# Kernel tuning notes

Measured on AMD Instinct MI355X. Metric: run time of the kernel, lower is better.

## Reference

```python
import jax, jax.numpy as jnp
import numpy as np

D_IN = 4096
D_OUT = 4096
RANK = 16
ALPHA = 32
SCALE = ALPHA / RANK


def setup_inputs() -> dict:
    key = jax.random.key(0)
    k_x, k_w, k_b, k_a = jax.random.split(key, 4)
    x = jax.random.normal(k_x, (4, 2048, D_IN), dtype=jnp.float32)
    weight = jax.random.normal(k_w, (D_OUT, D_IN), dtype=jnp.float32) * (1.0 / np.sqrt(D_IN))
    bias = jax.random.normal(k_b, (D_OUT,), dtype=jnp.float32)
    lora_A = jax.random.normal(k_a, (RANK, D_IN), dtype=jnp.float32) * 0.01
    lora_B = jnp.zeros((D_OUT, RANK), dtype=jnp.float32)
    return {"x": x, "weight": weight, "bias": bias, "lora_A": lora_A, "lora_B": lora_B}


def reference(x, weight, bias, lora_A, lora_B):
    # base linear: y = x @ W^T + b   -> [B, S, D_OUT]
    orig_out = jnp.einsum("bsd,od->bso", x, weight) + bias
    # low-rank path: (x @ A^T) @ B^T * (alpha/rank)
    lora_out = jnp.einsum("bsr,or->bso", jnp.einsum("bsd,rd->bsr", x, lora_A), lora_B)
    return orig_out + lora_out * SCALE
```

## Files before the change

### kernel.cpp

```cpp
#include <hip/hip_runtime.h>
#include <stdint.h>

#define DIN   4096
#define DOUT  4096
#define RANK  16
#define MTOT  8192
#define LSCALE 2.0f

typedef unsigned short u16;
typedef __bf16 bf16x8 __attribute__((ext_vector_type(8)));
typedef float  f32x4  __attribute__((ext_vector_type(4)));
typedef u16    u16x8  __attribute__((ext_vector_type(8)));

__device__ __forceinline__ u16 f2bf(float f) {
    uint32_t u = __builtin_bit_cast(uint32_t, f);
    u = (u + 0x7FFFu + ((u >> 16) & 1u)) >> 16;
    return (u16)u;
}

__device__ __forceinline__ u16x8 pack8(f32x4 a, f32x4 b) {
    u16x8 o;
    o[0] = f2bf(a[0]); o[1] = f2bf(a[1]); o[2] = f2bf(a[2]); o[3] = f2bf(a[3]);
    o[4] = f2bf(b[0]); o[5] = f2bf(b[1]); o[6] = f2bf(b[2]); o[7] = f2bf(b[3]);
    return o;
}

#define GLDS16(g, l) __builtin_amdgcn_global_load_lds( \
    (const __attribute__((address_space(1))) void*)(g), \
    (__attribute__((address_space(3))) void*)(l), 16, 0, 0)

__global__ __launch_bounds__(256) void k_convert_x(const float* __restrict__ x,
                                                   u16* __restrict__ xb) {
    long i = ((long)blockIdx.x * 256 + threadIdx.x) * 8;
    f32x4 a = *(const f32x4*)(x + i);
    f32x4 b = *(const f32x4*)(x + i + 4);
    *(u16x8*)(xb + i) = pack8(a, b);
}

__global__ __launch_bounds__(256) void k_build_weff(const float* __restrict__ W,
                                                    const float* __restrict__ A,
                                                    const float* __restrict__ B,
                                                    u16* __restrict__ wb) {
    long t = (long)blockIdx.x * 256 + threadIdx.x;
    long i = t * 8;
    int o = (int)(i >> 12);
    int d = (int)(i & (DIN - 1));
    float sB[RANK];
#pragma unroll
    for (int r = 0; r < RANK; ++r) sB[r] = B[o * RANK + r] * LSCALE;
    f32x4 w0 = *(const f32x4*)(W + i);
    f32x4 w1 = *(const f32x4*)(W + i + 4);
#pragma unroll
    for (int r = 0; r < RANK; ++r) {
        f32x4 a0 = *(const f32x4*)(A + (long)r * DIN + d);
        f32x4 a1 = *(const f32x4*)(A + (long)r * DIN + d + 4);
        w0 += a0 * sB[r];
        w1 += a1 * sB[r];
    }
    *(u16x8*)(wb + i) = pack8(w0, w1);
}

#define BM 256
#define BN 256
#define BK 64
#define NT (DIN / BK)

#define MFMA16(d, a, b) d = __builtin_amdgcn_mfma_f32_16x16x32_bf16(a, b, d, 0, 0, 0)
#define ABAR()   asm volatile("s_barrier" ::: "memory")
#define GATE4()  asm volatile("s_waitcnt vmcnt(4)" ::: "memory")
#define PRIO1()  __builtin_amdgcn_s_setprio(1)
#define PRIO0()  __builtin_amdgcn_s_setprio(0)

#define QUADK(mo, no, AF, BF) \
    _Pragma("unroll") \
    for (int kk = 0; kk < 2; ++kk) { \
        _Pragma("unroll") \
        for (int m = 0; m < 4; ++m) { \
            _Pragma("unroll") \
            for (int n = 0; n < 2; ++n) { \
                MFMA16(acc[(mo)+m][(no)+n], AF[m][kk], BF[n][kk]); \
            } \
        } \
    }

__global__ __launch_bounds__(512, 2) void k_gemm_ws(const u16* __restrict__ xb,
                                                    const u16* __restrict__ wb,
                                                    const float* __restrict__ bias,
                                                    float* __restrict__ out) {
    constexpr int K = DIN, N = DOUT;
    __shared__ alignas(16) u16 lds[65536];

    const int nchunk = gridDim.x >> 3;
    const int bid = blockIdx.x;
    const int wg  = (bid & 7) * nchunk + (bid >> 3);
    const int bm  = (wg & 31) * BM;
    const int bn  = (wg >> 5) * BN;

    const int tid  = threadIdx.x;
    const int lane = tid & 63;
    const int wid  = tid >> 6;
    const int wr   = wid >> 2;
    const int wc   = wid & 3;
    const int lrow = lane & 15;
    const int kgrp = lane >> 4;

    const int srow = tid >> 3;
    const int sgl  = (tid & 7) ^ (srow & 7);
    const u16* const aSrcB = xb + (long)(bm + srow) * K + sgl * 8;
    const u16* const bSrcB = wb + (long)(bn + srow) * K + sgl * 8;

#define STAGE_A(c, buf, kt) GLDS16(aSrcB + (long)(64*(c))*K + (kt)*BK, \
                                   lds + (buf)*16384 + (c)*4096 + tid*8)
#define STAGE_B(c, buf, kt) GLDS16(bSrcB + (long)(64*(c))*K + (kt)*BK, \
                                   lds + 32768 + (buf)*16384 + (c)*4096 + tid*8)

    const int go0 = (kgrp ^ (lrow & 7)) * 8;
    const int go1 = go0 ^ 32;
    const int arow = (wr*128 + lrow) * 64;
    const int brow = (wc*64  + lrow) * 64;

    f32x4 acc[8][4];
#pragma unroll
    for (int m = 0; m < 8; ++m)
#pragma unroll
        for (int n = 0; n < 4; ++n) acc[m][n] = (f32x4){0.f, 0.f, 0.f, 0.f};

    bf16x8 afL[4][2], afH[4][2], bfLo[2][2], bfHi[2][2];

    STAGE_A(0, 0, 0); STAGE_A(1, 0, 0);
    STAGE_A(2, 0, 0); STAGE_A(3, 0, 0);
    STAGE_B(0, 0, 0); STAGE_B(1, 0, 0);
    STAGE_B(2, 0, 0); STAGE_B(3, 0, 0);
    STAGE_B(0, 1, 1); STAGE_B(1, 1, 1);
    STAGE_B(2, 1, 1); STAGE_B(3, 1, 1);
    GATE4();
    __syncthreads();
#pragma unroll
    for (int nf = 0; nf < 2; ++nf) {
        const u16* b = lds + 32768 + brow + nf * 1024;
        bfLo[nf][0] = *(const bf16x8*)(b + go0);
        bfLo[nf][1] = *(const bf16x8*)(b + go1);
    }

    for (int t = 0; t < NT; ++t) {
        const int cur = t & 1, nxt = cur ^ 1;
        const int kt1 = (t + 1) & (NT - 1);
        const int kt2 = (t + 2) & (NT - 1);
        const u16* const cA = lds + cur * 16384;
        const u16* const cB = lds + 32768 + cur * 16384;
        const u16* const nB = lds + 32768 + nxt * 16384;

        STAGE_A(0, nxt, kt1); STAGE_A(1, nxt, kt1);
#pragma unroll
        for (int mf = 0; mf < 4; ++mf) {
            const u16* b = cA + arow + mf * 1024;
            afL[mf][0] = *(const bf16x8*)(b + go0);
            afL[mf][1] = *(const bf16x8*)(b + go1);
        }
        PRIO1(); QUADK(0, 0, afL, bfLo); PRIO0();
        ABAR();

        STAGE_A(2, nxt, kt1); STAGE_A(3, nxt, kt1);
#pragma unroll
        for (int nf = 0; nf < 2; ++nf) {
            const u16* b = cB + brow + (nf + 2) * 1024;
            bfHi[nf][0] = *(const bf16x8*)(b + go0);
            bfHi[nf][1] = *(const bf16x8*)(b + go1);
        }
        PRIO1(); QUADK(0, 2, afL, bfHi); PRIO0();
        ABAR();

        STAGE_B(0, cur, kt2); STAGE_B(1, cur, kt2);
#pragma unroll
        for (int mf = 0; mf < 4; ++mf) {
            const u16* b = cA + arow + (mf + 4) * 1024;
            afH[mf][0] = *(const bf16x8*)(b + go0);
            afH[mf][1] = *(const bf16x8*)(b + go1);
        }
        PRIO1(); QUADK(4, 0, afH, bfLo); PRIO0();
        ABAR();

        STAGE_B(2, cur, kt2); STAGE_B(3, cur, kt2);
        GATE4();
#pragma unroll
        for (int nf = 0; nf < 2; ++nf) {
            const u16* b = nB + brow + nf * 1024;
            bfLo[nf][0] = *(const bf16x8*)(b + go0);
            bfLo[nf][1] = *(const bf16x8*)(b + go1);
        }
        PRIO1(); QUADK(4, 2, afH, bfHi); PRIO0();
        ABAR();
    }
    asm volatile("s_waitcnt vmcnt(0)" ::: "memory");

    const int orow = bm + wr*128 + kgrp*4;
    const int ocol = bn + wc*64 + lrow;
#pragma unroll
    for (int n = 0; n < 4; ++n) {
        const int col = ocol + n*16;
        const float bj = bias[col];
#pragma unroll
        for (int m = 0; m < 8; ++m) {
            const int row = orow + m*16;
#pragma unroll
            for (int r = 0; r < 4; ++r)
                out[(long)(row + r) * N + col] = acc[m][n][r] + bj;
        }
    }
}

__global__ __launch_bounds__(64) void k_lora_T(const float* __restrict__ x,
                                               const float* __restrict__ A,
                                               float* __restrict__ T) {
    const int m = blockIdx.x;
    const int lane = threadIdx.x;
    const float* xr = x + (long)m * DIN;
    float acc[RANK];
#pragma unroll
    for (int r = 0; r < RANK; ++r) acc[r] = 0.f;
    for (int k = lane * 4; k < DIN; k += 64 * 4) {
        f32x4 xv = *(const f32x4*)(xr + k);
#pragma unroll
        for (int r = 0; r < RANK; ++r) {
            f32x4 av = *(const f32x4*)(A + (long)r * DIN + k);
            acc[r] += xv[0] * av[0] + xv[1] * av[1] + xv[2] * av[2] + xv[3] * av[3];
        }
    }
#pragma unroll
    for (int r = 0; r < RANK; ++r)
        for (int off = 32; off > 0; off >>= 1) acc[r] += __shfl_down(acc[r], off);
    if (lane == 0) {
#pragma unroll
        for (int r = 0; r < RANK; ++r) T[(long)m * RANK + r] = acc[r] * LSCALE;
    }
}

__global__ __launch_bounds__(256) void k_gemm_nows(const float* __restrict__ x,
                                                   const float* __restrict__ W,
                                                   const float* __restrict__ bias,
                                                   const float* __restrict__ T,
                                                   const float* __restrict__ lB,
                                                   float* __restrict__ out) {
    constexpr int FBM = 128, FBN = 128, FBK = 32, K = DIN, N = DOUT;
    __shared__ __align__(16) u16 As[FBM * FBK];
    __shared__ __align__(16) u16 Bs[FBN * FBK];

    const int tid = threadIdx.x;
    const int bm = blockIdx.y * FBM;
    const int bn = blockIdx.x * FBN;
    const int lane = tid & 63;
    const int wid  = tid >> 6;
    const int wr = wid >> 1, wc = wid & 1;
    const int lrow = lane & 15;
    const int kgrp = lane >> 4;

    const int c0 = tid, c1 = tid + 256;
    const float* aS0 = x + (long)(bm + (c0 >> 2)) * K + (c0 & 3) * 8;
    const float* aS1 = x + (long)(bm + (c1 >> 2)) * K + (c1 & 3) * 8;
    const float* bS0 = W + (long)(bn + (c0 >> 2)) * K + (c0 & 3) * 8;
    const float* bS1 = W + (long)(bn + (c1 >> 2)) * K + (c1 & 3) * 8;
    u16* aD0 = As + c0 * 8;  u16* aD1 = As + c1 * 8;
    u16* bD0 = Bs + c0 * 8;  u16* bD1 = Bs + c1 * 8;

    const u16* aR = As + (wr * 64 + lrow) * FBK + kgrp * 8;
    const u16* bR = Bs + (wc * 64 + lrow) * FBK + kgrp * 8;

    f32x4 acc[4][4];
#pragma unroll
    for (int i = 0; i < 4; ++i)
#pragma unroll
        for (int j = 0; j < 4; ++j) acc[i][j] = (f32x4){0.f, 0.f, 0.f, 0.f};

    for (int k0 = 0; k0 < K; k0 += FBK) {
        f32x4 a00 = *(const f32x4*)aS0, a01 = *(const f32x4*)(aS0 + 4);
        f32x4 a10 = *(const f32x4*)aS1, a11 = *(const f32x4*)(aS1 + 4);
        f32x4 b00 = *(const f32x4*)bS0, b01 = *(const f32x4*)(bS0 + 4);
        f32x4 b10 = *(const f32x4*)bS1, b11 = *(const f32x4*)(bS1 + 4);
        aS0 += FBK; aS1 += FBK; bS0 += FBK; bS1 += FBK;
        if (k0) __syncthreads();
        *(u16x8*)aD0 = pack8(a00, a01);
        *(u16x8*)aD1 = pack8(a10, a11);
        *(u16x8*)bD0 = pack8(b00, b01);
        *(u16x8*)bD1 = pack8(b10, b11);
        __syncthreads();

        bf16x8 af[4], bf[4];
#pragma unroll
        for (int i = 0; i < 4; ++i) af[i] = *(const bf16x8*)(aR + i * 16 * FBK);
#pragma unroll
        for (int j = 0; j < 4; ++j) bf[j] = *(const bf16x8*)(bR + j * 16 * FBK);
#pragma unroll
        for (int i = 0; i < 4; ++i)
#pragma unroll
            for (int j = 0; j < 4; ++j)
                acc[i][j] = __builtin_amdgcn_mfma_f32_16x16x32_bf16(af[i], bf[j], acc[i][j], 0, 0, 0);
    }

#pragma unroll
    for (int j = 0; j < 4; ++j) {
        const int col = bn + wc * 64 + j * 16 + lrow;
        const float bj = bias[col];
        float bl[RANK];
#pragma unroll
        for (int q = 0; q < RANK; ++q) bl[q] = lB[(long)col * RANK + q];
#pragma unroll
        for (int i = 0; i < 4; ++i) {
            const int row0 = bm + wr * 64 + i * 16 + kgrp * 4;
#pragma unroll
            for (int r = 0; r < 4; ++r) {
                const int row = row0 + r;
                const float* Trow = T + (long)row * RANK;
                float s = bj;
#pragma unroll
                for (int q = 0; q < RANK; ++q) s += Trow[q] * bl[q];
                out[(long)row * N + col] = acc[i][j][r] + s;
            }
        }
    }
}

extern "C" void kernel_launch(void* const* d_in, const int* in_sizes, int n_in,
                              void* d_out, int out_size, void* d_ws, size_t ws_size,
                              hipStream_t stream) {
    const float* x    = (const float*)d_in[0];
    const float* W    = (const float*)d_in[1];
    const float* bias = (const float*)d_in[2];
    const float* lA   = (const float*)d_in[3];
    const float* lB   = (const float*)d_in[4];
    float* out = (float*)d_out;

    const size_t xb_bytes = (size_t)MTOT * DIN * sizeof(u16);
    const size_t wb_bytes = (size_t)DOUT * DIN * sizeof(u16);

    if (ws_size >= xb_bytes + wb_bytes) {
        u16* xb = (u16*)d_ws;
        u16* wb = (u16*)((char*)d_ws + xb_bytes);
        k_convert_x <<<(int)((long)MTOT * DIN / 8 / 256), 256, 0, stream>>>(x, xb);
        k_build_weff<<<(int)((long)DOUT * DIN / 8 / 256), 256, 0, stream>>>(W, lA, lB, wb);
        k_gemm_ws   <<<(MTOT / BM) * (DOUT / BN), 512, 0, stream>>>(xb, wb, bias, out);
    } else {
        float* T = (float*)d_ws;
        k_lora_T   <<<MTOT, 64, 0, stream>>>(x, lA, T);
        k_gemm_nows<<<dim3(DOUT / 128, MTOT / 128), 256, 0, stream>>>(x, W, bias, T, lB, out);
    }
}
```

Before: 329.8 us.

## Load GEMM B operand straight from global into registers, halving LDS staging

Weight (B) tiles are no longer staged through LDS. Each wave now loads its B fragments directly from global memory into double-buffered registers, and only the X (A) tile is staged in an LDS ping-pong buffer, which halves LDS use. The k-loop is unrolled by two, with each sub-step running all four N fragments against both M halves. This cuts LDS traffic and barriers, but adds redundant, less coalesced global loads of W, more register pressure, and reads LDS after only a per-wave vmcnt wait with no barrier, which risks a cross-wave race.

Result: slower. 455.3 us (+38.1%).

```diff
diff --git a/kernel.cpp b/kernel.cpp
--- a/kernel.cpp
+++ b/kernel.cpp
@@ -67,19 +67,28 @@
 
 #define MFMA16(d, a, b) d = __builtin_amdgcn_mfma_f32_16x16x32_bf16(a, b, d, 0, 0, 0)
 #define ABAR()   asm volatile("s_barrier" ::: "memory")
-#define GATE4()  asm volatile("s_waitcnt vmcnt(4)" ::: "memory")
+#define GATE12() asm volatile("s_waitcnt vmcnt(12)" ::: "memory")
 #define PRIO1()  __builtin_amdgcn_s_setprio(1)
 #define PRIO0()  __builtin_amdgcn_s_setprio(0)
 
-#define QUADK(mo, no, AF, BF) \
+#define QUADB(mo, AF, BF) \
     _Pragma("unroll") \
     for (int kk = 0; kk < 2; ++kk) { \
         _Pragma("unroll") \
         for (int m = 0; m < 4; ++m) { \
             _Pragma("unroll") \
-            for (int n = 0; n < 2; ++n) { \
-                MFMA16(acc[(mo)+m][(no)+n], AF[m][kk], BF[n][kk]); \
+            for (int n = 0; n < 4; ++n) { \
+                MFMA16(acc[(mo)+m][n], AF[m][kk], BF[n][kk]); \
             } \
+        } \
+    }
+
+#define LOADB(DST, kt) \
+    _Pragma("unroll") \
+    for (int nf = 0; nf < 4; ++nf) { \
+        _Pragma("unroll") \
+        for (int kk = 0; kk < 2; ++kk) { \
+            DST[nf][kk] = *(const bf16x8*)(bRow + (long)nf*16*K + (kt)*BK + kk*32); \
         } \
     }
 
@@ -88,7 +97,7 @@
                                                     const float* __restrict__ bias,
                                                     float* __restrict__ out) {
     constexpr int K = DIN, N = DOUT;
-    __shared__ alignas(16) u16 lds[65536];
+    __shared__ alignas(16) u16 lds[32768];
 
     const int nchunk = gridDim.x >> 3;
     const int bid = blockIdx.x;
@@ -107,17 +116,15 @@
     const int srow = tid >> 3;
     const int sgl  = (tid & 7) ^ (srow & 7);
     const u16* const aSrcB = xb + (long)(bm + srow) * K + sgl * 8;
-    const u16* const bSrcB = wb + (long)(bn + srow) * K + sgl * 8;
 
 #define STAGE_A(c, buf, kt) GLDS16(aSrcB + (long)(64*(c))*K + (kt)*BK, \
                                    lds + (buf)*16384 + (c)*4096 + tid*8)
-#define STAGE_B(c, buf, kt) GLDS16(bSrcB + (long)(64*(c))*K + (kt)*BK, \
-                                   lds + 32768 + (buf)*16384 + (c)*4096 + tid*8)
 
     const int go0 = (kgrp ^ (lrow & 7)) * 8;
     const int go1 = go0 ^ 32;
     const int arow = (wr*128 + lrow) * 64;
-    const int brow = (wc*64  + lrow) * 64;
+
+    const u16* const bRow = wb + (long)(bn + wc*64 + lrow) * K + kgrp * 8;
 
     f32x4 acc[8][4];
 #pragma unroll
@@ -125,70 +132,56 @@
 #pragma unroll
         for (int n = 0; n < 4; ++n) acc[m][n] = (f32x4){0.f, 0.f, 0.f, 0.f};
 
-    bf16x8 afL[4][2], afH[4][2], bfLo[2][2], bfHi[2][2];
+    bf16x8 afL[4][2], afH[4][2], bE[4][2], bO[4][2];
 
     STAGE_A(0, 0, 0); STAGE_A(1, 0, 0);
     STAGE_A(2, 0, 0); STAGE_A(3, 0, 0);
-    STAGE_B(0, 0, 0); STAGE_B(1, 0, 0);
-    STAGE_B(2, 0, 0); STAGE_B(3, 0, 0);
-    STAGE_B(0, 1, 1); STAGE_B(1, 1, 1);
-    STAGE_B(2, 1, 1); STAGE_B(3, 1, 1);
-    GATE4();
+    LOADB(bE, 0);
+    asm volatile("s_waitcnt vmcnt(0)" ::: "memory");
     __syncthreads();
-#pragma unroll
-    for (int nf = 0; nf < 2; ++nf) {
-        const u16* b = lds + 32768 + brow + nf * 1024;
-        bfLo[nf][0] = *(const bf16x8*)(b + go0);
-        bfLo[nf][1] = *(const bf16x8*)(b + go1);
-    }
-
-    for (int t = 0; t < NT; ++t) {
-        const int cur = t & 1, nxt = cur ^ 1;
-        const int kt1 = (t + 1) & (NT - 1);
+
+    for (int it = 0; it < NT/2; ++it) {
+        const int t   = 2*it;
+        const int kt1 = t + 1;
         const int kt2 = (t + 2) & (NT - 1);
-        const u16* const cA = lds + cur * 16384;
-        const u16* const cB = lds + 32768 + cur * 16384;
-        const u16* const nB = lds + 32768 + nxt * 16384;
-
-        STAGE_A(0, nxt, kt1); STAGE_A(1, nxt, kt1);
+
+        LOADB(bO, kt1);
+        STAGE_A(0, 1, kt1); STAGE_A(1, 1, kt1);
+        STAGE_A(2, 1, kt1); STAGE_A(3, 1, kt1);
+        GATE12();
 #pragma unroll
         for (int mf = 0; mf < 4; ++mf) {
-            const u16* b = cA + arow + mf * 1024;
+            const u16* b = lds + arow + mf * 1024;
             afL[mf][0] = *(const bf16x8*)(b + go0);
             afL[mf][1] = *(const bf16x8*)(b + go1);
         }
-        PRIO1(); QUADK(0, 0, afL, bfLo); PRIO0();
-        ABAR();
-
-        STAGE_A(2, nxt, kt1); STAGE_A(3, nxt, kt1);
-#pragma unroll
-        for (int nf = 0; nf < 2; ++nf) {
-            const u16* b = cB + brow + (nf + 2) * 1024;
-            bfHi[nf][0] = *(const bf16x8*)(b + go0);
-            bfHi[nf][1] = *(const bf16x8*)(b + go1);
-        }
-        PRIO1(); QUADK(0, 2, afL, bfHi); PRIO0();
-        ABAR();
-
-        STAGE_B(0, cur, kt2); STAGE_B(1, cur, kt2);
+        PRIO1(); QUADB(0, afL, bE); PRIO0();
 #pragma unroll
         for (int mf = 0; mf < 4; ++mf) {
-            const u16* b = cA + arow + (mf + 4) * 1024;
+            const u16* b = lds + arow + (mf + 4) * 1024;
             afH[mf][0] = *(const bf16x8*)(b + go0);
             afH[mf][1] = *(const bf16x8*)(b + go1);
         }
-        PRIO1(); QUADK(4, 0, afH, bfLo); PRIO0();
+        PRIO1(); QUADB(4, afH, bE); PRIO0();
         ABAR();
-
-        STAGE_B(2, cur, kt2); STAGE_B(3, cur, kt2);
-        GATE4();
-#pragma unroll
-        for (int nf = 0; nf < 2; ++nf) {
-            const u16* b = nB + brow + nf * 1024;
-            bfLo[nf][0] = *(const bf16x8*)(b + go0);
-            bfLo[nf][1] = *(const bf16x8*)(b + go1);
-        }
-        PRIO1(); QUADK(4, 2, afH, bfHi); PRIO0();
+        LOADB(bE, kt2);
+        STAGE_A(0, 0, kt2); STAGE_A(1, 0, kt2);
+        STAGE_A(2, 0, kt2); STAGE_A(3, 0, kt2);
+        GATE12();
+#pragma unroll
+        for (int mf = 0; mf < 4; ++mf) {
+            const u16* b = lds + 16384 + arow + mf * 1024;
+            afL[mf][0] = *(const bf16x8*)(b + go0);
+            afL[mf][1] = *(const bf16x8*)(b + go1);
+        }
+        PRIO1(); QUADB(0, afL, bO); PRIO0();
+#pragma unroll
+        for (int mf = 0; mf < 4; ++mf) {
+            const u16* b = lds + 16384 + arow + (mf + 4) * 1024;
+            afH[mf][0] = *(const bf16x8*)(b + go0);
+            afH[mf][1] = *(const bf16x8*)(b + go1);
+        }
+        PRIO1(); QUADB(4, afH, bO); PRIO0();
         ABAR();
     }
     asm volatile("s_waitcnt vmcnt(0)" ::: "memory");
```

## Reuse LoRA A rows across output rows and restructure GEMM main loop

Applied to the files above, without the earlier changes.

The W_eff build kernel now loads the 16 LoRA A vectors for a column chunk into registers once. It then loops over 16 output rows, instead of reloading A for every row, which cuts redundant cache traffic. The GEMM main loop is unrolled by two k-tiles with fixed LDS buffer pointers. Each phase now issues all four A (or B) staging loads together and merges the two MFMA quads per phase, removing per-iteration buffer index arithmetic. The cost is that load/compute overlap is reshaped and register pressure rises from the extra B fragment set.

Result: faster. 290.0 us (median of 2 runs) (-12.1%).

```diff
diff --git a/kernel.cpp b/kernel.cpp
--- a/kernel.cpp
+++ b/kernel.cpp
@@ -37,27 +37,35 @@
     *(u16x8*)(xb + i) = pack8(a, b);
 }
 
+#define WEFF_OPG 16
 __global__ __launch_bounds__(256) void k_build_weff(const float* __restrict__ W,
                                                     const float* __restrict__ A,
                                                     const float* __restrict__ B,
                                                     u16* __restrict__ wb) {
-    long t = (long)blockIdx.x * 256 + threadIdx.x;
-    long i = t * 8;
-    int o = (int)(i >> 12);
-    int d = (int)(i & (DIN - 1));
-    float sB[RANK];
-#pragma unroll
-    for (int r = 0; r < RANK; ++r) sB[r] = B[o * RANK + r] * LSCALE;
-    f32x4 w0 = *(const f32x4*)(W + i);
-    f32x4 w1 = *(const f32x4*)(W + i + 4);
+    const long t = (long)blockIdx.x * 256 + threadIdx.x;
+    const int dc = (int)(t & 511);
+    const int og = (int)(t >> 9);
+    const int d  = dc * 8;
+    f32x4 a0[RANK], a1[RANK];
 #pragma unroll
     for (int r = 0; r < RANK; ++r) {
-        f32x4 a0 = *(const f32x4*)(A + (long)r * DIN + d);
-        f32x4 a1 = *(const f32x4*)(A + (long)r * DIN + d + 4);
-        w0 += a0 * sB[r];
-        w1 += a1 * sB[r];
-    }
-    *(u16x8*)(wb + i) = pack8(w0, w1);
+        a0[r] = *(const f32x4*)(A + (long)r * DIN + d);
+        a1[r] = *(const f32x4*)(A + (long)r * DIN + d + 4);
+    }
+#pragma unroll 4
+    for (int j = 0; j < WEFF_OPG; ++j) {
+        const int o = og * WEFF_OPG + j;
+        const long i = (long)o * DIN + d;
+        f32x4 w0 = *(const f32x4*)(W + i);
+        f32x4 w1 = *(const f32x4*)(W + i + 4);
+#pragma unroll
+        for (int r = 0; r < RANK; ++r) {
+            const float s = B[o * RANK + r] * LSCALE;
+            w0 += a0[r] * s;
+            w1 += a1[r] * s;
+        }
+        *(u16x8*)(wb + i) = pack8(w0, w1);
+    }
 }
 
 #define BM 256
@@ -119,13 +127,33 @@
     const int arow = (wr*128 + lrow) * 64;
     const int brow = (wc*64  + lrow) * 64;
 
+    const u16* const cA0 = lds +         arow;
+    const u16* const cA1 = lds + 16384 + arow;
+    const u16* const cB0 = lds + 32768 +         brow;
+    const u16* const cB1 = lds + 32768 + 16384 + brow;
+
     f32x4 acc[8][4];
 #pragma unroll
     for (int m = 0; m < 8; ++m)
 #pragma unroll
         for (int n = 0; n < 4; ++n) acc[m][n] = (f32x4){0.f, 0.f, 0.f, 0.f};
 
-    bf16x8 afL[4][2], afH[4][2], bfLo[2][2], bfHi[2][2];
+    bf16x8 afL[4][2], afH[4][2], bfHi[2][2], bLoA[2][2], bLoB[2][2];
+
+#define READ_AF(DST, BASE, OFS) \
+    _Pragma("unroll") \
+    for (int mf = 0; mf < 4; ++mf) { \
+        const u16* b_ = (BASE) + ((OFS) + mf) * 1024; \
+        DST[mf][0] = *(const bf16x8*)(b_ + go0); \
+        DST[mf][1] = *(const bf16x8*)(b_ + go1); \
+    }
+#define READ_BF(DST, BASE, OFS) \
+    _Pragma("unroll") \
+    for (int nf = 0; nf < 2; ++nf) { \
+        const u16* b_ = (BASE) + ((OFS) + nf) * 1024; \
+        DST[nf][0] = *(const bf16x8*)(b_ + go0); \
+        DST[nf][1] = *(const bf16x8*)(b_ + go1); \
+    }
 
     STAGE_A(0, 0, 0); STAGE_A(1, 0, 0);
     STAGE_A(2, 0, 0); STAGE_A(3, 0, 0);
@@ -135,60 +163,40 @@
     STAGE_B(2, 1, 1); STAGE_B(3, 1, 1);
     GATE4();
     __syncthreads();
-#pragma unroll
-    for (int nf = 0; nf < 2; ++nf) {
-        const u16* b = lds + 32768 + brow + nf * 1024;
-        bfLo[nf][0] = *(const bf16x8*)(b + go0);
-        bfLo[nf][1] = *(const bf16x8*)(b + go1);
-    }
-
-    for (int t = 0; t < NT; ++t) {
-        const int cur = t & 1, nxt = cur ^ 1;
-        const int kt1 = (t + 1) & (NT - 1);
-        const int kt2 = (t + 2) & (NT - 1);
-        const u16* const cA = lds + cur * 16384;
-        const u16* const cB = lds + 32768 + cur * 16384;
-        const u16* const nB = lds + 32768 + nxt * 16384;
-
-        STAGE_A(0, nxt, kt1); STAGE_A(1, nxt, kt1);
-#pragma unroll
-        for (int mf = 0; mf < 4; ++mf) {
-            const u16* b = cA + arow + mf * 1024;
-            afL[mf][0] = *(const bf16x8*)(b + go0);
-            afL[mf][1] = *(const bf16x8*)(b + go1);
-        }
-        PRIO1(); QUADK(0, 0, afL, bfLo); PRIO0();
+    READ_BF(bLoA, cB0, 0);
+
+    for (int it = 0; it < NT/2; ++it) {
+        const int kt1 = 2*it + 1;
+        const int kt2 = (2*it + 2) & (NT - 1);
+        const int kt3 = (2*it + 3) & (NT - 1);
+
+        STAGE_A(0, 1, kt1); STAGE_A(1, 1, kt1);
+        STAGE_A(2, 1, kt1); STAGE_A(3, 1, kt1);
+        READ_AF(afL, cA0, 0);
+        READ_BF(bfHi, cB0, 2);
+        PRIO1(); QUADK(0, 0, afL, bLoA); QUADK(0, 2, afL, bfHi); PRIO0();
         ABAR();
-
-        STAGE_A(2, nxt, kt1); STAGE_A(3, nxt, kt1);
-#pragma unroll
-        for (int nf = 0; nf < 2; ++nf) {
-            const u16* b = cB + brow + (nf + 2) * 1024;
-            bfHi[nf][0] = *(const bf16x8*)(b + go0);
-            bfHi[nf][1] = *(const bf16x8*)(b + go1);
-        }
-        PRIO1(); QUADK(0, 2, afL, bfHi); PRIO0();
+        STAGE_B(0, 0, kt2); STAGE_B(1, 0, kt2);
+        STAGE_B(2, 0, kt2); STAGE_B(3, 0, kt2);
+        GATE4();
+        READ_AF(afH, cA0, 4);
+        READ_BF(bLoB, cB1, 0);
+        PRIO1(); QUADK(4, 0, afH, bLoA); QUADK(4, 2, afH, bfHi); PRIO0();
         ABAR();
 
-        STAGE_B(0, cur, kt2); STAGE_B(1, cur, kt2);
-#pragma unroll
-        for (int mf = 0; mf < 4; ++mf) {
-            const u16* b = cA + arow + (mf + 4) * 1024;
-            afH[mf][0] = *(const bf16x8*)(b + go0);
-            afH[mf][1] = *(const bf16x8*)(b + go1);
-        }
-        PRIO1(); QUADK(4, 0, afH, bfLo); PRIO0();
+        STAGE_A(0, 0, kt2); STAGE_A(1, 0, kt2);
+        STAGE_A(2, 0, kt2); STAGE_A(3, 0, kt2);
+        READ_AF(afL, cA1, 0);
+        READ_BF(bfHi, cB1, 2);
+        PRIO1(); QUADK(0, 0, afL, bLoB); QUADK(0, 2, afL, bfHi); PRIO0();
         ABAR();
 
-        STAGE_B(2, cur, kt2); STAGE_B(3, cur, kt2);
+        STAGE_B(0, 1, kt3); STAGE_B(1, 1, kt3);
+        STAGE_B(2, 1, kt3); STAGE_B(3, 1, kt3);
         GATE4();
-#pragma unroll
-        for (int nf = 0; nf < 2; ++nf) {
-            const u16* b = nB + brow + nf * 1024;
-            bfLo[nf][0] = *(const bf16x8*)(b + go0);
-            bfLo[nf][1] = *(const bf16x8*)(b + go1);
-        }
-        PRIO1(); QUADK(4, 2, afH, bfHi); PRIO0();
+        READ_AF(afH, cA1, 4);
+        READ_BF(bLoA, cB0, 0);
+        PRIO1(); QUADK(4, 0, afH, bLoB); QUADK(4, 2, afH, bfHi); PRIO0();
         ABAR();
     }
     asm volatile("s_waitcnt vmcnt(0)" ::: "memory");
@@ -336,7 +344,7 @@
         u16* xb = (u16*)d_ws;
         u16* wb = (u16*)((char*)d_ws + xb_bytes);
         k_convert_x <<<(int)((long)MTOT * DIN / 8 / 256), 256, 0, stream>>>(x, xb);
-        k_build_weff<<<(int)((long)DOUT * DIN / 8 / 256), 256, 0, stream>>>(W, lA, lB, wb);
+        k_build_weff<<<(DOUT / WEFF_OPG) * (DIN / 8) / 256, 256, 0, stream>>>(W, lA, lB, wb);
         k_gemm_ws   <<<(MTOT / BM) * (DOUT / BN), 512, 0, stream>>>(xb, wb, bias, out);
     } else {
         float* T = (float*)d_ws;
```
